# Performance work log

Hardware: AMD Instinct MI355X
Metric: run time of the kernel (lower is better)

The kernel has to match this reference:

```python
import jax, jax.numpy as jnp
import numpy as np

B, T, H, P = 512, 256, 256, 14  # batch, seq_len, hidden_size, predict_seq


def _lstm_layer(x_tbf, w_ih, w_hh, b_ih, b_hh):
    """One LSTM layer. x_tbf: [T, B, F]. Returns outputs [T, B, H].
    PyTorch gate order: i, f, g, o."""
    # Precompute input contribution for all timesteps: [T, B, 4H]
    pre = jnp.einsum('tbf,gf->tbg', x_tbf, w_ih) + b_ih + b_hh
    h0 = jnp.zeros((x_tbf.shape[1], w_hh.shape[1]), dtype=x_tbf.dtype)
    c0 = jnp.zeros_like(h0)

    def step(carry, pre_t):
        h, c = carry
        gates = pre_t + h @ w_hh.T                      # [B, 4H]
        i, f, g, o = jnp.split(gates, 4, axis=-1)
        i = jax.nn.sigmoid(i)
        f = jax.nn.sigmoid(f)
        g = jnp.tanh(g)
        o = jax.nn.sigmoid(o)
        c = f * c + i * g
        h = o * jnp.tanh(c)
        return (h, c), h

    _, ys = jax.lax.scan(step, (h0, c0), pre)
    return ys  # [T, B, H]


def setup_inputs() -> dict:
    key = jax.random.key(0)
    ks = jax.random.split(key, 11)
    s = 1.0 / np.sqrt(H)  # torch LSTM/Linear default init scale
    return {
        'x':     jax.random.normal(ks[0], (B, T, 1), dtype=jnp.float32),
        'w_ih0': jax.random.uniform(ks[1], (4 * H, 1), jnp.float32, -s, s),
        'w_hh0': jax.random.uniform(ks[2], (4 * H, H), jnp.float32, -s, s),
        'b_ih0': jax.random.uniform(ks[3], (4 * H,), jnp.float32, -s, s),
        'b_hh0': jax.random.uniform(ks[4], (4 * H,), jnp.float32, -s, s),
        'w_ih1': jax.random.uniform(ks[5], (4 * H, H), jnp.float32, -s, s),
        'w_hh1': jax.random.uniform(ks[6], (4 * H, H), jnp.float32, -s, s),
        'b_ih1': jax.random.uniform(ks[7], (4 * H,), jnp.float32, -s, s),
        'b_hh1': jax.random.uniform(ks[8], (4 * H,), jnp.float32, -s, s),
        'w_lin': jax.random.uniform(ks[9], (P, H), jnp.float32, -s, s),
        'b_lin': jax.random.uniform(ks[10], (P,), jnp.float32, -s, s),
    }


def reference(x, w_ih0, w_hh0, b_ih0, b_hh0, w_ih1, w_hh1, b_ih1, b_hh1,
              w_lin, b_lin):
    xt = jnp.transpose(x, (1, 0, 2))                 # [T, B, 1]
    h1 = _lstm_layer(xt, w_ih0, w_hh0, b_ih0, b_hh0)  # [T, B, H]
    h2 = _lstm_layer(h1, w_ih1, w_hh1, b_ih1, b_hh1)  # [T, B, H]
    last = h2[-1]                                     # [B, H] == x[:, -1, :]
    return last @ w_lin.T + b_lin                     # [B, P]
```

## Files before the change

### kernel.cpp

```cpp
#include <hip/hip_runtime.h>

constexpr int Bz = 512;
constexpr int Tz = 256;
constexpr int Hz = 256;
constexpr int Pz = 14;
constexpr int GB = 32;
constexpr int GS = 8;
constexpr int BT = 16;
constexpr int KP = 264;
constexpr int XS = 260;

typedef short s8v __attribute__((ext_vector_type(8)));
typedef float f4v __attribute__((ext_vector_type(4)));
typedef unsigned long long u64;

__device__ __forceinline__ short f2bf(float f) {
  unsigned u = __float_as_uint(f);
  u = (u + 0x7fffu + ((u >> 16) & 1u)) >> 16;
  return (short)u;
}
__device__ __forceinline__ float bf2f(short s) {
  return __uint_as_float(((unsigned)(unsigned short)s) << 16);
}
__device__ __forceinline__ float sigm(float v) {
  return __builtin_amdgcn_rcpf(1.0f + __builtin_amdgcn_exp2f(-1.442695041f * v));
}
__device__ __forceinline__ float tanh_f(float v) {
  return 1.0f - 2.0f * __builtin_amdgcn_rcpf(__builtin_amdgcn_exp2f(2.885390082f * v) + 1.0f);
}

__device__ __forceinline__ u64 llc_load64(const u64* p) {
  return __hip_atomic_load(p, __ATOMIC_RELAXED, __HIP_MEMORY_SCOPE_AGENT);
}
__device__ __forceinline__ unsigned llc_load32(const unsigned* p) {
  return __hip_atomic_load(p, __ATOMIC_RELAXED, __HIP_MEMORY_SCOPE_AGENT);
}
__device__ __forceinline__ void llc_store32(unsigned* p, unsigned v) {
  __hip_atomic_store(p, v, __ATOMIC_RELAXED, __HIP_MEMORY_SCOPE_AGENT);
}
__device__ __forceinline__ void llc_store64(u64* p, u64 v) {
  __hip_atomic_store(p, v, __ATOMIC_RELAXED, __HIP_MEMORY_SCOPE_AGENT);
}

__global__ void __launch_bounds__(256, 1)
lstm2(const float* __restrict__ x,
      const float* __restrict__ w_ih0, const float* __restrict__ w_hh0,
      const float* __restrict__ b_ih0, const float* __restrict__ b_hh0,
      const float* __restrict__ w_ih1, const float* __restrict__ w_hh1,
      const float* __restrict__ b_ih1, const float* __restrict__ b_hh1,
      const float* __restrict__ w_lin, const float* __restrict__ b_lin,
      float* __restrict__ out,
      u64* __restrict__ hg, unsigned* __restrict__ flags)
{
  const int blk  = blockIdx.x;
  const int g    = blk >> 3;
  const int sl   = blk & 7;
  const int tid  = threadIdx.x;
  const int w    = tid >> 6;
  const int lane = tid & 63;
  const int q    = lane >> 4;
  const int l15  = lane & 15;
  const int gbase = g * BT;

  extern __shared__ char smem_raw[];
  short* h0s = (short*)smem_raw;
  short* h1s = h0s + BT * KP;
  float* xls = (float*)(h1s + BT * KP);
  float* wls = xls + BT * XS;

  s8v Wf[3][2][8];
  {
    const float* wsrc[3] = {w_hh0, w_ih1, w_hh1};
    #pragma unroll
    for (int mat = 0; mat < 3; ++mat) {
      #pragma unroll
      for (int mti = 0; mti < 2; ++mti) {
        int rr = (w + mti * 4) * 16 + l15;
        int grow = (rr & 3) * Hz + sl * 32 + (rr >> 2);
        const float* p = wsrc[mat] + (size_t)grow * Hz;
        #pragma unroll
        for (int kt = 0; kt < 8; ++kt) {
          s8v f;
          #pragma unroll
          for (int j = 0; j < 8; ++j) {
            int ktrue = kt * 32 + q * 4 + (j >> 1) + 16 * (j & 1);
            f[j] = f2bf(p[ktrue]);
          }
          Wf[mat][mti][kt] = f;
        }
      }
    }
  }
  const int uA = w * 4 + q, uB = 16 + w * 4 + q;
  float wihA[4], wihB[4], b0A[4], b0B[4], b1A[4], b1B[4];
  #pragma unroll
  for (int r = 0; r < 4; ++r) {
    int ga_ = r * Hz + sl * 32 + uA;
    int gb_ = r * Hz + sl * 32 + uB;
    wihA[r] = w_ih0[ga_];              wihB[r] = w_ih0[gb_];
    b0A[r]  = b_ih0[ga_] + b_hh0[ga_]; b0B[r]  = b_ih0[gb_] + b_hh0[gb_];
    b1A[r]  = b_ih1[ga_] + b_hh1[ga_]; b1B[r]  = b_ih1[gb_] + b_hh1[gb_];
  }
  float c0A = 0.f, c0B = 0.f, c1A = 0.f, c1B = 0.f;

  for (int i = tid; i < BT * (Tz / 4); i += 256) {
    int b = i >> 6, c4 = i & 63;
    f4v v = *(const f4v*)(x + (size_t)(gbase + b) * Tz + c4 * 4);
    *(f4v*)(xls + b * XS + c4 * 4) = v;
  }
  if (sl == 0) {
    for (int i = tid; i < Pz * Hz; i += 256) {
      int p = i >> 8, kpos = i & 255;
      int sl2 = kpos >> 5, w2 = (kpos >> 3) & 3, q2 = (kpos >> 1) & 3, jj = kpos & 1;
      wls[i] = w_lin[p * Hz + sl2 * 32 + w2 * 4 + q2 + 16 * jj];
    }
  }

  const unsigned* myflags = flags + g * 32 + (lane & 7);
  unsigned* myflag = flags + g * 32 + sl;

  for (int s = 0; s <= Tz; ++s) {
    if (w == 0) {
      const unsigned expd = (unsigned)s;
      unsigned f = llc_load32(myflags);
      while (__ballot(f >= expd) != ~0ull) {
        __builtin_amdgcn_s_sleep(1);
        f = llc_load32(myflags);
      }
    }
    __syncthreads();

    {
      const u64* sp = hg + (size_t)((s + 1) & 1) * 65536;
      u64 r[8];
      #pragma unroll
      for (int k = 0; k < 4; ++k) {
        int i = tid + k * 256;
        int c = i & 1, b = (i >> 1) & 15, slw = i >> 5;
        size_t gi = ((size_t)slw * Bz + gbase + b) * 4 + 2 * c;
        r[2 * k]     = llc_load64(sp + gi);
        r[2 * k + 1] = llc_load64(sp + gi + 1);
      }
      #pragma unroll
      for (int k = 0; k < 4; ++k) {
        int i = tid + k * 256;
        int c = i & 1, b = (i >> 1) & 15, slw = i >> 5;
        u64 lo = r[2 * k], hi = r[2 * k + 1];
        *(u64*)(h0s + b * KP + slw * 8 + c * 4) =
            (u64)(unsigned)lo | ((u64)(unsigned)hi << 32);
        *(u64*)(h1s + b * KP + slw * 8 + c * 4) =
            (lo >> 32) | ((hi >> 32) << 32);
      }
    }
    __syncthreads();

    f4v a0A = {0.f,0.f,0.f,0.f}, a0B = {0.f,0.f,0.f,0.f};
    f4v a1A = {0.f,0.f,0.f,0.f}, a1B = {0.f,0.f,0.f,0.f};
    const short* H0f = h0s + l15 * KP + q * 8;
    const short* H1f = h1s + l15 * KP + q * 8;
    #pragma unroll
    for (int kt = 0; kt < 8; ++kt) {
      s8v h0v = *(const s8v*)(H0f + kt * 32);
      s8v h1v = *(const s8v*)(H1f + kt * 32);
      a0A = __builtin_amdgcn_mfma_f32_16x16x32_bf16(Wf[0][0][kt], h0v, a0A, 0, 0, 0);
      a0B = __builtin_amdgcn_mfma_f32_16x16x32_bf16(Wf[0][1][kt], h0v, a0B, 0, 0, 0);
      a1A = __builtin_amdgcn_mfma_f32_16x16x32_bf16(Wf[1][0][kt], h0v, a1A, 0, 0, 0);
      a1B = __builtin_amdgcn_mfma_f32_16x16x32_bf16(Wf[1][1][kt], h0v, a1B, 0, 0, 0);
      a1A = __builtin_amdgcn_mfma_f32_16x16x32_bf16(Wf[2][0][kt], h1v, a1A, 0, 0, 0);
      a1B = __builtin_amdgcn_mfma_f32_16x16x32_bf16(Wf[2][1][kt], h1v, a1B, 0, 0, 0);
    }

    unsigned pk0 = 0, pk1 = 0;
    if (s < Tz) {
      float xv = xls[l15 * XS + s];
      float iA = sigm  (a0A[0] + xv * wihA[0] + b0A[0]);
      float fA = sigm  (a0A[1] + xv * wihA[1] + b0A[1]);
      float gA = tanh_f(a0A[2] + xv * wihA[2] + b0A[2]);
      float oA = sigm  (a0A[3] + xv * wihA[3] + b0A[3]);
      c0A = fA * c0A + iA * gA;
      float iB = sigm  (a0B[0] + xv * wihB[0] + b0B[0]);
      float fB = sigm  (a0B[1] + xv * wihB[1] + b0B[1]);
      float gB = tanh_f(a0B[2] + xv * wihB[2] + b0B[2]);
      float oB = sigm  (a0B[3] + xv * wihB[3] + b0B[3]);
      c0B = fB * c0B + iB * gB;
      pk0 = (unsigned)(unsigned short)f2bf(oA * tanh_f(c0A))
          | ((unsigned)(unsigned short)f2bf(oB * tanh_f(c0B)) << 16);
    }
    if (s >= 1) {
      float iA = sigm  (a1A[0] + b1A[0]);
      float fA = sigm  (a1A[1] + b1A[1]);
      float gA = tanh_f(a1A[2] + b1A[2]);
      float oA = sigm  (a1A[3] + b1A[3]);
      c1A = fA * c1A + iA * gA;
      float iB = sigm  (a1B[0] + b1B[0]);
      float fB = sigm  (a1B[1] + b1B[1]);
      float gB = tanh_f(a1B[2] + b1B[2]);
      float oB = sigm  (a1B[3] + b1B[3]);
      c1B = fB * c1B + iB * gB;
      pk1 = (unsigned)(unsigned short)f2bf(oA * tanh_f(c1A))
          | ((unsigned)(unsigned short)f2bf(oB * tanh_f(c1B)) << 16);
    }

    {
      size_t base = (size_t)(sl * 4 + w) * 2048 + (size_t)(gbase + l15) * 4 + q;
      llc_store64(hg + (size_t)(s & 1) * 65536 + base,
                  (u64)pk0 | ((u64)pk1 << 32));
    }

    __syncthreads();
    if (tid == 0)
      llc_store32(myflag, (unsigned)(s + 1));
  }

  if (sl == 0) {
    {
      const unsigned expd = (unsigned)(Tz + 1);
      unsigned f = llc_load32(myflags);
      while (__ballot(f >= expd) != ~0ull) {
        __builtin_amdgcn_s_sleep(1);
        f = llc_load32(myflags);
      }
    }
    const u64* sp = hg + (size_t)(Tz & 1) * 65536;
    for (int k = 0; k < 4; ++k) {
      int i = tid + k * 256;
      int c = i & 1, b = (i >> 1) & 15, slw = i >> 5;
      size_t gi = ((size_t)slw * Bz + gbase + b) * 4 + 2 * c;
      u64 lo = llc_load64(sp + gi);
      u64 hi = llc_load64(sp + gi + 1);
      *(u64*)(h0s + b * KP + slw * 8 + c * 4) = (lo >> 32) | ((hi >> 32) << 32);
    }
    __syncthreads();
    for (int i = tid; i < BT * Pz; i += 256) {
      int b = i / Pz, p = i - b * Pz;
      const float* wr = wls + p * Hz;
      float acc = b_lin[p];
      for (int kk = 0; kk < Hz; ++kk)
        acc += bf2f(h0s[b * KP + kk]) * wr[kk];
      out[(gbase + b) * Pz + p] = acc;
    }
  }
}

extern "C" void kernel_launch(void* const* d_in, const int* in_sizes, int n_in,
                              void* d_out, int out_size, void* d_ws, size_t ws_size,
                              hipStream_t stream) {
  const float* x     = (const float*)d_in[0];
  const float* w_ih0 = (const float*)d_in[1];
  const float* w_hh0 = (const float*)d_in[2];
  const float* b_ih0 = (const float*)d_in[3];
  const float* b_hh0 = (const float*)d_in[4];
  const float* w_ih1 = (const float*)d_in[5];
  const float* w_hh1 = (const float*)d_in[6];
  const float* b_ih1 = (const float*)d_in[7];
  const float* b_hh1 = (const float*)d_in[8];
  const float* w_lin = (const float*)d_in[9];
  const float* b_lin = (const float*)d_in[10];
  float* out = (float*)d_out;

  unsigned char* ws = (unsigned char*)d_ws;
  u64* hg         = (u64*)ws;
  unsigned* flags = (unsigned*)(ws + (1 << 20));
  hipMemsetAsync(d_ws, 0, (1 << 20) + 4096, stream);

  size_t lds_bytes = (size_t)(2 * BT) * KP * 2
                   + (size_t)(BT * XS) * 4
                   + (size_t)(Pz * Hz) * 4;
  hipFuncSetAttribute((const void*)lstm2,
                      hipFuncAttributeMaxDynamicSharedMemorySize, (int)lds_bytes);
  lstm2<<<GB * GS, 256, lds_bytes, stream>>>(x, w_ih0, w_hh0, b_ih0, b_hh0,
                                             w_ih1, w_hh1, b_ih1, b_hh1,
                                             w_lin, b_lin, out, hg, flags);
}
```

Measured before the change: 727.5 us.

## Issue hidden-state loads before the flag wait and validate them with embedded parity bits

The global loads of the previous step's hidden state are now issued before waiting on the inter-block flag. Each load is then checked against a parity bit stored in the low mantissa bit of the layer-1 value, and only stale entries are reloaded. This overlaps load latency with the barrier wait and precomputes the address arithmetic once, outside the loop. The cost is one bit of bf16 precision in layer-1 h, plus extra polling loops that could spin when data arrives late.

```diff
diff --git a/kernel.cpp b/kernel.cpp
--- a/kernel.cpp
+++ b/kernel.cpp
@@ -116,10 +116,27 @@
     }
   }
 
+  size_t gidx[8];
+  int ldo[4];
+  #pragma unroll
+  for (int k = 0; k < 4; ++k) {
+    int i = tid + k * 256;
+    int c = i & 1, b = (i >> 1) & 15, slw = i >> 5;
+    gidx[2 * k]     = ((size_t)slw * Bz + gbase + b) * 4 + 2 * c;
+    gidx[2 * k + 1] = gidx[2 * k] + 1;
+    ldo[k] = b * KP + slw * 8 + c * 4;
+  }
+  const size_t stbase = (size_t)(sl * 4 + w) * 2048 + (size_t)(gbase + l15) * 4 + q;
+
   const unsigned* myflags = flags + g * 32 + (lane & 7);
   unsigned* myflag = flags + g * 32 + sl;
 
   for (int s = 0; s <= Tz; ++s) {
+    const u64* sp = hg + (size_t)((s + 1) & 1) * 65536;
+    u64 v[8];
+    #pragma unroll
+    for (int j = 0; j < 8; ++j) v[j] = llc_load64(sp + gidx[j]);
+
     if (w == 0) {
       const unsigned expd = (unsigned)s;
       unsigned f = llc_load32(myflags);
@@ -131,26 +148,25 @@
     __syncthreads();
 
     {
-      const u64* sp = hg + (size_t)((s + 1) & 1) * 65536;
-      u64 r[8];
-      #pragma unroll
-      for (int k = 0; k < 4; ++k) {
-        int i = tid + k * 256;
-        int c = i & 1, b = (i >> 1) & 15, slw = i >> 5;
-        size_t gi = ((size_t)slw * Bz + gbase + b) * 4 + 2 * c;
-        r[2 * k]     = llc_load64(sp + gi);
-        r[2 * k + 1] = llc_load64(sp + gi + 1);
-      }
-      #pragma unroll
-      for (int k = 0; k < 4; ++k) {
-        int i = tid + k * 256;
-        int c = i & 1, b = (i >> 1) & 15, slw = i >> 5;
-        u64 lo = r[2 * k], hi = r[2 * k + 1];
-        *(u64*)(h0s + b * KP + slw * 8 + c * 4) =
-            (u64)(unsigned)lo | ((u64)(unsigned)hi << 32);
-        *(u64*)(h1s + b * KP + slw * 8 + c * 4) =
-            (lo >> 32) | ((hi >> 32) << 32);
-      }
+      const unsigned expb = (s == 0) ? 0u
+                          : ((((unsigned)(s - 1) >> 1) & 1u) ^ 1u);
+      for (;;) {
+        unsigned miss = 0;
+        #pragma unroll
+        for (int j = 0; j < 8; ++j)
+          if ((unsigned)((v[j] >> 32) & 1u) != expb) miss |= 1u << j;
+        if (!miss) break;
+        #pragma unroll
+        for (int j = 0; j < 8; ++j)
+          if (miss & (1u << j)) v[j] = llc_load64(sp + gidx[j]);
+        __builtin_amdgcn_s_sleep(2);
+      }
+    }
+    #pragma unroll
+    for (int k = 0; k < 4; ++k) {
+      u64 lo = v[2 * k], hi = v[2 * k + 1];
+      *(u64*)(h0s + ldo[k]) = (u64)(unsigned)lo | ((u64)(unsigned)hi << 32);
+      *(u64*)(h1s + ldo[k]) = (lo >> 32) | ((hi >> 32) << 32);
     }
     __syncthreads();
 
@@ -200,12 +216,10 @@
       pk1 = (unsigned)(unsigned short)f2bf(oA * tanh_f(c1A))
           | ((unsigned)(unsigned short)f2bf(oB * tanh_f(c1B)) << 16);
     }
-
-    {
-      size_t base = (size_t)(sl * 4 + w) * 2048 + (size_t)(gbase + l15) * 4 + q;
-      llc_store64(hg + (size_t)(s & 1) * 65536 + base,
-                  (u64)pk0 | ((u64)pk1 << 32));
-    }
+    pk1 = (pk1 & ~1u) | ((((unsigned)s >> 1) & 1u) ^ 1u);
+
+    llc_store64(hg + (size_t)(s & 1) * 65536 + stbase,
+                (u64)pk0 | ((u64)pk1 << 32));
 
     __syncthreads();
     if (tid == 0)
@@ -223,12 +237,9 @@
     }
     const u64* sp = hg + (size_t)(Tz & 1) * 65536;
     for (int k = 0; k < 4; ++k) {
-      int i = tid + k * 256;
-      int c = i & 1, b = (i >> 1) & 15, slw = i >> 5;
-      size_t gi = ((size_t)slw * Bz + gbase + b) * 4 + 2 * c;
-      u64 lo = llc_load64(sp + gi);
-      u64 hi = llc_load64(sp + gi + 1);
-      *(u64*)(h0s + b * KP + slw * 8 + c * 4) = (lo >> 32) | ((hi >> 32) << 32);
+      u64 lo = llc_load64(sp + gidx[2 * k]);
+      u64 hi = llc_load64(sp + gidx[2 * k + 1]);
+      *(u64*)(h0s + ldo[k]) = (lo >> 32) | ((hi >> 32) << 32);
     }
     __syncthreads();
     for (int i = tid; i < BT * Pz; i += 256) {
```

Result: slower. 830.4 us (+14.2%).
